# Optimization experiments

Hardware: AMD Instinct MI355X
Metric: run time of the kernel (lower is better)

Reference implementation:

```python
import jax, jax.numpy as jnp
import numpy as np

DIM = 112        # input channels
DIM_OUT = 224    # output channels (stage transition)
HEADS = 4
HD = DIM_OUT // HEADS          # 56
WS = 8                         # window size before query pooling
QS = 2                         # query_stride
MLP_DIM = int(DIM_OUT * 4.0)   # 896
EPS = 1e-6
SCALE = HD ** -0.5


def _layernorm(x, g, b):
    m = x.mean(-1, keepdims=True)
    d = x - m
    v = (d * d).mean(-1, keepdims=True)
    return d * jax.lax.rsqrt(v + EPS) * g + b


def _maxpool2(x):
    # stride==pool_size max pooling via reshape (NHWC)
    B, H, W, C = x.shape
    return x.reshape(B, H // QS, QS, W // QS, QS, C).max(axis=(2, 4))


def setup_inputs() -> dict:
    key = jax.random.key(0)
    ks = jax.random.split(key, 8)
    def n(k, s, sc=0.02):
        return jax.random.normal(k, s, dtype=jnp.float32) * sc
    return {
        "hidden_states": jax.random.normal(ks[0], (8, 128, 128, DIM), dtype=jnp.float32),
        "ln1_g": jnp.ones((DIM,), jnp.float32),
        "ln1_b": jnp.zeros((DIM,), jnp.float32),
        "qkv_w": n(ks[1], (DIM, 3 * DIM_OUT)),
        "qkv_b": jnp.zeros((3 * DIM_OUT,), jnp.float32),
        "attn_proj_w": n(ks[2], (DIM_OUT, DIM_OUT)),
        "attn_proj_b": jnp.zeros((DIM_OUT,), jnp.float32),
        "res_proj_w": n(ks[3], (DIM, DIM_OUT)),
        "res_proj_b": jnp.zeros((DIM_OUT,), jnp.float32),
        "ln2_g": jnp.ones((DIM_OUT,), jnp.float32),
        "ln2_b": jnp.zeros((DIM_OUT,), jnp.float32),
        "mlp1_w": n(ks[4], (DIM_OUT, MLP_DIM)),
        "mlp1_b": jnp.zeros((MLP_DIM,), jnp.float32),
        "mlp2_w": n(ks[5], (MLP_DIM, DIM_OUT)),
        "mlp2_b": jnp.zeros((DIM_OUT,), jnp.float32),
    }


def reference(hidden_states, ln1_g, ln1_b, qkv_w, qkv_b, attn_proj_w, attn_proj_b,
              res_proj_w, res_proj_b, ln2_g, ln2_b, mlp1_w, mlp1_b, mlp2_w, mlp2_b):
    x = hidden_states
    B, H, W, _ = x.shape  # H, W divisible by WS -> no padding branch needed
    hs = _layernorm(x, ln1_g, ln1_b)
    # dim != dim_out: residual = pooled projection of normed input
    residual = _maxpool2(hs @ res_proj_w + res_proj_b)  # (B, H/2, W/2, DIM_OUT)

    # window partition: (B*nh*nw, WS, WS, DIM)
    nh, nw = H // WS, W // WS
    w = hs.reshape(B, nh, WS, nw, WS, DIM).transpose(0, 1, 3, 2, 4, 5)
    w = w.reshape(B * nh * nw, WS, WS, DIM)

    # multi-scale attention with query pooling
    qkv = (w @ qkv_w + qkv_b).reshape(-1, WS * WS, 3, HEADS, HD)
    q, k, v = qkv[:, :, 0], qkv[:, :, 1], qkv[:, :, 2]
    q = _maxpool2(q.reshape(-1, WS, WS, DIM_OUT))          # (Bw, WS/2, WS/2, DIM_OUT)
    q = q.reshape(-1, (WS // QS) ** 2, HEADS, HD)
    q = q.transpose(0, 2, 1, 3)   # (Bw, h, Lq, d)
    k = k.transpose(0, 2, 1, 3)   # (Bw, h, Lk, d)
    v = v.transpose(0, 2, 1, 3)
    attn = jax.nn.softmax(jnp.einsum('bhqd,bhkd->bhqk', q * SCALE, k), axis=-1)
    o = jnp.einsum('bhqk,bhkd->bhqd', attn, v).transpose(0, 2, 1, 3)
    ws2 = WS // QS
    o = o.reshape(-1, ws2, ws2, DIM_OUT)
    o = o @ attn_proj_w + attn_proj_b

    # window unpartition at pooled resolution
    H2, W2 = H // QS, W // QS
    o = o.reshape(B, nh, nw, ws2, ws2, DIM_OUT).transpose(0, 1, 3, 2, 4, 5)
    o = o.reshape(B, H2, W2, DIM_OUT)

    hs = residual + o
    ln = _layernorm(hs, ln2_g, ln2_b)
    mlp = jax.nn.gelu(ln @ mlp1_w + mlp1_b, approximate=False) @ mlp2_w + mlp2_b
    return hs + mlp
```

## Files before the change

### kernel.cpp

```cpp
#include <hip/hip_runtime.h>
#include <hip/hip_bf16.h>
#include <math.h>


#define SCALE_A 0.13363062095621219f

typedef __attribute__((ext_vector_type(8))) short short8;
typedef __attribute__((ext_vector_type(4))) short short4v;
typedef __attribute__((ext_vector_type(4))) float f32x4;
typedef __attribute__((ext_vector_type(16))) float f32x16;

__device__ inline short f2bf(float x) {
  union { float f; unsigned u; } v; v.f = x;
  unsigned r = v.u + 0x7fff + ((v.u >> 16) & 1);
  return (short)(r >> 16);
}
__device__ inline float gelu_fast(float x) {
  float x2 = x * x;
  float p = fmaf(x2, 0.044715f, 1.0f);
  float t = -1.5957691216057308f * x * p;
  return x / (1.0f + __expf(t));
}

__global__ void cast_w_kernel(const float* __restrict__ qkv_w,
                              const float* __restrict__ rp_w,
                              const float* __restrict__ ap_w,
                              const float* __restrict__ m1_w,
                              const float* __restrict__ m2_w,
                              short* __restrict__ wF) {
  int tid = blockIdx.x * blockDim.x + threadIdx.x;
  int stride = gridDim.x * blockDim.x;
  for (int e = tid; e < 90112; e += stride) {
    int j = e & 7, lr = (e >> 3) & 15, lqq = (e >> 7) & 3, tile = e >> 9;
    int kt = tile & 3, nt = tile >> 2;
    int cp = nt * 16 + lr;
    int h = cp / 176, cl = cp % 176;
    int k = kt * 32 + lqq * 8 + j;
    float val = 0.f;
    if (k < 112 && cl < 168) {
      int bcol = (cl < 56) ? (h * 56 + cl)
               : (cl < 112) ? (224 + h * 56 + (cl - 56))
                            : (448 + h * 56 + (cl - 112));
      val = qkv_w[k * 672 + bcol];
    }
    wF[e] = f2bf(val);
  }
  for (int e = tid; e < 28672; e += stride) {
    int j = e & 7, lr = (e >> 3) & 15, lqq = (e >> 7) & 3, tile = e >> 9;
    int kt = tile & 3, nt = tile >> 2;
    int n = nt * 16 + lr, k = kt * 32 + lqq * 8 + j;
    wF[90112 + e] = (k < 112) ? f2bf(rp_w[k * 224 + n]) : (short)0;
  }
  for (int e = tid; e < 50176; e += stride) {
    int j = e & 7, lr = (e >> 3) & 15, lqq = (e >> 7) & 3, tile = e >> 9;
    int kt = tile % 7, nt = tile / 7;
    int n = nt * 16 + lr, k = kt * 32 + lqq * 8 + j;
    wF[118784 + e] = f2bf(ap_w[k * 224 + n]);
  }
  for (int e = tid; e < 200704; e += stride) {
    int j = e & 7, lane = (e >> 3) & 63, unit = e >> 9;
    int kt = unit % 14, nt = unit / 14;
    int n = nt * 32 + (lane & 31), k = kt * 16 + (lane >> 5) * 8 + j;
    wF[168960 + e] = f2bf(m1_w[k * 896 + n]);
  }
  for (int e = tid; e < 200704; e += stride) {
    int j = e & 7, lane = (e >> 3) & 63, unit = e >> 9;
    int kt = unit % 56, nt = unit / 56;
    int n = nt * 32 + (lane & 31), k = kt * 16 + (lane >> 5) * 8 + j;
    wF[369664 + e] = f2bf(m2_w[k * 224 + n]);
  }
}

__global__ __launch_bounds__(256) void ln1_kernel(
    const float* __restrict__ x, const float* __restrict__ g,
    const float* __restrict__ b, short* __restrict__ hs) {
  int wave = threadIdx.x >> 6, lane = threadIdx.x & 63;
  int half = lane >> 5, sub = lane & 31;
  size_t row = (size_t)blockIdx.x * 8 + wave * 2 + half;
  const float* rp = x + row * 112;
  f32x4 v = {0.f, 0.f, 0.f, 0.f};
  if (sub < 28) v = *(const f32x4*)(rp + sub * 4);
  float s = v[0] + v[1] + v[2] + v[3];
  #pragma unroll
  for (int off = 16; off; off >>= 1) s += __shfl_xor(s, off, 32);
  float mean = s * (1.f / 112.f);
  float s2 = 0.f;
  #pragma unroll
  for (int q = 0; q < 4; ++q) { float d = v[q] - mean; s2 = fmaf(d, d, s2); }
  if (sub >= 28) s2 = 0.f;
  #pragma unroll
  for (int off = 16; off; off >>= 1) s2 += __shfl_xor(s2, off, 32);
  float rs = rsqrtf(s2 * (1.f / 112.f) + 1e-6f);
  if (sub < 28) {
    f32x4 gg = *(const f32x4*)(g + sub * 4);
    f32x4 bb = *(const f32x4*)(b + sub * 4);
    short4v o;
    #pragma unroll
    for (int q = 0; q < 4; ++q)
      o[q] = f2bf((v[q] - mean) * rs * gg[q] + bb[q]);
    *(short4v*)(hs + row * 112 + sub * 4) = o;
  }
}

__global__ __launch_bounds__(256, 8) void respool_kernel(
    const short* __restrict__ hs, const short* __restrict__ rpF,
    const float* __restrict__ bias, float* __restrict__ hs2) {
  __shared__ alignas(16) short w_s[64 * 136];
  int blk = blockIdx.x;
  int tid = threadIdx.x;
  for (int e = tid; e < 1024; e += 256) {
    int m = e >> 4, c = e & 15;
    short8* dst = (short8*)&w_s[m * 136 + c * 8];
    if (c < 14) {
      int p = m >> 2, r = m & 3;
      int pix = blk * 16 + p;
      int bb = pix >> 12, ii = (pix >> 6) & 63, jj = pix & 63;
      size_t token = ((size_t)(bb * 128 + 2 * ii + (r >> 1))) * 128 + 2 * jj + (r & 1);
      *dst = *(const short8*)(hs + token * 112 + c * 8);
    } else {
      short8 z = {0, 0, 0, 0, 0, 0, 0, 0};
      *dst = z;
    }
  }
  __syncthreads();
  int wave = tid >> 6, lane = tid & 63, lrow = lane & 15, lq = lane >> 4;
  short8 Ar[4];
  #pragma unroll
  for (int kt = 0; kt < 4; ++kt)
    Ar[kt] = *(const short8*)&w_s[(wave * 16 + lrow) * 136 + kt * 32 + lq * 8];
  int p = wave * 4 + lq;
  for (int pr = 0; pr < 7; ++pr) {
    int c0 = pr * 32 + lrow, c1 = c0 + 16;
    f32x4 acc0 = {0.f, 0.f, 0.f, 0.f}, acc1 = {0.f, 0.f, 0.f, 0.f};
    #pragma unroll
    for (int kt = 0; kt < 4; ++kt) {
      short8 b0 = *(const short8*)(rpF + (((2 * pr) * 4 + kt) * 64 + lane) * 8);
      short8 b1 = *(const short8*)(rpF + (((2 * pr + 1) * 4 + kt) * 64 + lane) * 8);
      acc0 = __builtin_amdgcn_mfma_f32_16x16x32_bf16(Ar[kt], b0, acc0, 0, 0, 0);
      acc1 = __builtin_amdgcn_mfma_f32_16x16x32_bf16(Ar[kt], b1, acc1, 0, 0, 0);
    }
    float m0 = fmaxf(fmaxf(acc0[0], acc0[1]), fmaxf(acc0[2], acc0[3])) + bias[c0];
    float m1 = fmaxf(fmaxf(acc1[0], acc1[1]), fmaxf(acc1[2], acc1[3])) + bias[c1];
    hs2[(size_t)(blk * 16 + p) * 224 + c0] = m0;
    hs2[(size_t)(blk * 16 + p) * 224 + c1] = m1;
  }
}

__global__ __launch_bounds__(256, 2) void attn_kernel(
    const short* __restrict__ hs, const short* __restrict__ qkvF,
    const float* __restrict__ qkv_b, short* __restrict__ o_bf) {
  __shared__ alignas(16) short u_s[4 * 9792];
  int win = blockIdx.x;
  int nw = win & 15, nh = (win >> 4) & 15, b = win >> 8;
  int tid = threadIdx.x;
  int wave = tid >> 6, lane = tid & 63, lrow = lane & 15, lq = lane >> 4;
  short* w_s  = u_s;
  short* k_s  = u_s + wave * 9792;
  short* vT_s = k_s + 4608;
  short* qp_s = k_s + 8640;

  for (int e = tid; e < 1024; e += 256) {
    int m = e >> 4, c = e & 15;
    short8* dst = (short8*)&w_s[m * 136 + c * 8];
    if (c < 14) {
      int p = m >> 2, r = m & 3;
      int tr = (p >> 2) * 2 + (r >> 1), tc = (p & 3) * 2 + (r & 1);
      size_t token = ((size_t)(b * 128 + nh * 8 + tr)) * 128 + (nw * 8 + tc);
      *dst = *(const short8*)(hs + token * 112 + c * 8);
    } else {
      short8 z = {0, 0, 0, 0, 0, 0, 0, 0};
      *dst = z;
    }
  }
  __syncthreads();

  short8 Aw[4][4];
  #pragma unroll
  for (int mt = 0; mt < 4; ++mt)
    #pragma unroll
    for (int kt = 0; kt < 4; ++kt)
      Aw[mt][kt] = *(const short8*)&w_s[(mt * 16 + lrow) * 136 + kt * 32 + lq * 8];
  __syncthreads();

  {
    short8 z = {0, 0, 0, 0, 0, 0, 0, 0};
    *(short8*)&k_s[lane * 72 + 56] = z;
    if (lane < 16) *(short8*)&qp_s[lane * 72 + 56] = z;
  }

  int h = wave;

  #pragma unroll 2
  for (int t = 0; t < 11; ++t) {
    int cl = t * 16 + lrow;
    f32x4 ac[4] = {{0.f,0.f,0.f,0.f},{0.f,0.f,0.f,0.f},
                   {0.f,0.f,0.f,0.f},{0.f,0.f,0.f,0.f}};
    short8 bw[4];
    #pragma unroll
    for (int kt = 0; kt < 4; ++kt)
      bw[kt] = *(const short8*)(qkvF + (((h * 11 + t) * 4 + kt) * 64 + lane) * 8);
    #pragma unroll
    for (int kt = 0; kt < 4; ++kt)
      #pragma unroll
      for (int mt = 0; mt < 4; ++mt)
        ac[mt] = __builtin_amdgcn_mfma_f32_16x16x32_bf16(Aw[mt][kt], bw[kt], ac[mt], 0, 0, 0);
    if (cl < 56) {
      float bias = qkv_b[h * 56 + cl];
      #pragma unroll
      for (int mt = 0; mt < 4; ++mt) {
        float mx = fmaxf(fmaxf(ac[mt][0], ac[mt][1]),
                         fmaxf(ac[mt][2], ac[mt][3])) + bias;
        qp_s[(mt * 4 + lq) * 72 + cl] = f2bf(mx * SCALE_A);
      }
    } else if (cl < 112) {
      float bias = qkv_b[224 + h * 56 + (cl - 56)];
      #pragma unroll
      for (int mt = 0; mt < 4; ++mt)
        #pragma unroll
        for (int r = 0; r < 4; ++r)
          k_s[(mt * 16 + lq * 4 + r) * 72 + (cl - 56)] = f2bf(ac[mt][r] + bias);
    } else if (cl < 168) {
      float bias = qkv_b[448 + h * 56 + (cl - 112)];
      #pragma unroll
      for (int mt = 0; mt < 4; ++mt) {
        short4v pk = {f2bf(ac[mt][0] + bias), f2bf(ac[mt][1] + bias),
                      f2bf(ac[mt][2] + bias), f2bf(ac[mt][3] + bias)};
        *(short4v*)&vT_s[(cl - 112) * 72 + mt * 16 + lq * 4] = pk;
      }
    }
  }

  short8 aq[2];
  #pragma unroll
  for (int kt = 0; kt < 2; ++kt)
    aq[kt] = *(const short8*)&qp_s[lrow * 72 + kt * 32 + lq * 8];
  f32x4 sc[4];
  #pragma unroll
  for (int t = 0; t < 4; ++t) {
    sc[t][0] = sc[t][1] = sc[t][2] = sc[t][3] = 0.f;
    #pragma unroll
    for (int kt = 0; kt < 2; ++kt) {
      short8 bk = *(const short8*)&k_s[(t * 16 + lrow) * 72 + kt * 32 + lq * 8];
      sc[t] = __builtin_amdgcn_mfma_f32_16x16x32_bf16(aq[kt], bk, sc[t], 0, 0, 0);
    }
  }
  float mr[4], sr[4];
  #pragma unroll
  for (int r = 0; r < 4; ++r)
    mr[r] = fmaxf(fmaxf(sc[0][r], sc[1][r]), fmaxf(sc[2][r], sc[3][r]));
  #pragma unroll
  for (int off = 8; off; off >>= 1)
    #pragma unroll
    for (int r = 0; r < 4; ++r) mr[r] = fmaxf(mr[r], __shfl_xor(mr[r], off, 16));
  #pragma unroll
  for (int r = 0; r < 4; ++r) {
    #pragma unroll
    for (int t = 0; t < 4; ++t) sc[t][r] = __expf(sc[t][r] - mr[r]);
    sr[r] = sc[0][r] + sc[1][r] + sc[2][r] + sc[3][r];
  }
  #pragma unroll
  for (int off = 8; off; off >>= 1)
    #pragma unroll
    for (int r = 0; r < 4; ++r) sr[r] += __shfl_xor(sr[r], off, 16);
  #pragma unroll
  for (int r = 0; r < 4; ++r) sr[r] = 1.f / sr[r];
  #pragma unroll
  for (int t = 0; t < 4; ++t)
    #pragma unroll
    for (int r = 0; r < 4; ++r)
      qp_s[(lq * 4 + r) * 72 + t * 16 + lrow] = f2bf(sc[t][r] * sr[r]);

  short8 ap[2];
  #pragma unroll
  for (int kt = 0; kt < 2; ++kt)
    ap[kt] = *(const short8*)&qp_s[lrow * 72 + kt * 32 + lq * 8];
  #pragma unroll
  for (int ct = 0; ct < 4; ++ct) {
    int c0 = (ct < 3) ? ct * 16 : 40;
    int col = c0 + lrow;
    f32x4 ov = {0.f, 0.f, 0.f, 0.f};
    #pragma unroll
    for (int kt = 0; kt < 2; ++kt) {
      short8 bv = *(const short8*)&vT_s[col * 72 + kt * 32 + lq * 8];
      ov = __builtin_amdgcn_mfma_f32_16x16x32_bf16(ap[kt], bv, ov, 0, 0, 0);
    }
    if (ct < 3 || lrow >= 8) {
      #pragma unroll
      for (int r = 0; r < 4; ++r) {
        int row = lq * 4 + r;
        size_t token = ((size_t)(b * 64 + nh * 4 + (row >> 2))) * 64 + (nw * 4 + (row & 3));
        o_bf[token * 224 + h * 56 + col] = f2bf(ov[r]);
      }
    }
  }
}

__global__ __launch_bounds__(256, 5) void aproj_kernel(
    const short* __restrict__ o_bf, const short* __restrict__ apF,
    const float* __restrict__ apb, float* __restrict__ hs2) {
  __shared__ alignas(16) short o_s[64 * 232];
  int blk = blockIdx.x;
  int tid = threadIdx.x;
  for (int e = tid; e < 64 * 28; e += 256) {
    int m = e / 28, c = e % 28;
    *(short8*)&o_s[m * 232 + c * 8] =
        *(const short8*)(o_bf + ((size_t)blk * 64 + m) * 224 + c * 8);
  }
  __syncthreads();
  int wave = tid >> 6, lane = tid & 63, lrow = lane & 15, lq = lane >> 4;
  short8 Ao[7];
  #pragma unroll
  for (int kt = 0; kt < 7; ++kt)
    Ao[kt] = *(const short8*)&o_s[(wave * 16 + lrow) * 232 + kt * 32 + lq * 8];
  for (int pr = 0; pr < 7; ++pr) {
    int c0 = pr * 32 + lrow, c1 = c0 + 16;
    f32x4 acc0 = {0.f, 0.f, 0.f, 0.f}, acc1 = {0.f, 0.f, 0.f, 0.f};
    #pragma unroll
    for (int kt = 0; kt < 7; ++kt) {
      short8 b0 = *(const short8*)(apF + (((2 * pr) * 7 + kt) * 64 + lane) * 8);
      short8 b1 = *(const short8*)(apF + (((2 * pr + 1) * 7 + kt) * 64 + lane) * 8);
      acc0 = __builtin_amdgcn_mfma_f32_16x16x32_bf16(Ao[kt], b0, acc0, 0, 0, 0);
      acc1 = __builtin_amdgcn_mfma_f32_16x16x32_bf16(Ao[kt], b1, acc1, 0, 0, 0);
    }
    float bi0 = apb[c0], bi1 = apb[c1];
    #pragma unroll
    for (int r = 0; r < 4; ++r) {
      size_t row = (size_t)blk * 64 + wave * 16 + lq * 4 + r;
      hs2[row * 224 + c0] += acc0[r] + bi0;
      hs2[row * 224 + c1] += acc1[r] + bi1;
    }
  }
}

template <int NT>
__device__ __forceinline__ void mlp1_tiles(
    int nt0, const short* ln_s, const short* __restrict__ m1F,
    const float* __restrict__ b1, short* hid_s, int nl, int half, int lane) {
  f32x16 acc[NT];
  #pragma unroll
  for (int i = 0; i < NT; ++i)
    #pragma unroll
    for (int r = 0; r < 16; ++r) acc[i][r] = 0.f;
  #pragma unroll
  for (int kt = 0; kt < 14; ++kt) {
    short8 a = *(const short8*)&ln_s[nl * 232 + kt * 16 + half * 8];
    #pragma unroll
    for (int i = 0; i < NT; ++i) {
      short8 bw = *(const short8*)(m1F + ((size_t)((nt0 + i) * 14 + kt) * 64 + lane) * 8);
      acc[i] = __builtin_amdgcn_mfma_f32_32x32x16_bf16(a, bw, acc[i], 0, 0, 0);
    }
  }
  #pragma unroll
  for (int i = 0; i < NT; ++i) {
    int col = (nt0 + i) * 32 + nl;
    float bi = b1[col];
    #pragma unroll
    for (int r = 0; r < 16; ++r) {
      int row = (r & 3) + 8 * (r >> 2) + 4 * half;
      hid_s[row * 904 + col] = f2bf(gelu_fast(acc[i][r] + bi));
    }
  }
}

__global__ __launch_bounds__(512, 4) void mlp_kernel(
    const float* __restrict__ hs2, const float* __restrict__ g2,
    const float* __restrict__ b2, const short* __restrict__ m1F,
    const float* __restrict__ b1, const short* __restrict__ m2F,
    const float* __restrict__ b2b, float* __restrict__ out) {
  __shared__ alignas(16) short ln_s[32 * 232];
  __shared__ alignas(16) short hid_s[32 * 904];
  int blk = blockIdx.x;
  int tid = threadIdx.x;
  size_t base = (size_t)blk * 32 * 224;
  {
    int row = tid >> 4, l = tid & 15;
    const float* rp = hs2 + base + (size_t)row * 224;
    float v[14];
    float s = 0.f;
    #pragma unroll
    for (int c = 0; c < 14; ++c) { v[c] = rp[l + 16 * c]; s += v[c]; }
    #pragma unroll
    for (int off = 8; off; off >>= 1) s += __shfl_xor(s, off, 16);
    float mean = s * (1.f / 224.f);
    float s2 = 0.f;
    #pragma unroll
    for (int c = 0; c < 14; ++c) { float d = v[c] - mean; s2 = fmaf(d, d, s2); }
    #pragma unroll
    for (int off = 8; off; off >>= 1) s2 += __shfl_xor(s2, off, 16);
    float rs = rsqrtf(s2 * (1.f / 224.f) + 1e-6f);
    #pragma unroll
    for (int c = 0; c < 14; ++c) {
      int cc = l + 16 * c;
      ln_s[row * 232 + cc] = f2bf((v[c] - mean) * rs * g2[cc] + b2[cc]);
    }
  }
  __syncthreads();
  int wave = tid >> 6, lane = tid & 63;
  int nl = lane & 31, half = lane >> 5;
  if (wave < 4) mlp1_tiles<4>(wave * 4, ln_s, m1F, b1, hid_s, nl, half, lane);
  else          mlp1_tiles<3>(16 + (wave - 4) * 3, ln_s, m1F, b1, hid_s, nl, half, lane);
  __syncthreads();
  if (wave < 7) {
    int nt = wave;
    int col = nt * 32 + nl;
    float res[16];
    #pragma unroll
    for (int r = 0; r < 16; ++r) {
      int row = (r & 3) + 8 * (r >> 2) + 4 * half;
      res[r] = hs2[base + (size_t)row * 224 + col];
    }
    f32x16 ac0 = {0.f,0.f,0.f,0.f,0.f,0.f,0.f,0.f,0.f,0.f,0.f,0.f,0.f,0.f,0.f,0.f};
    f32x16 ac1 = {0.f,0.f,0.f,0.f,0.f,0.f,0.f,0.f,0.f,0.f,0.f,0.f,0.f,0.f,0.f,0.f};
    #pragma unroll 4
    for (int kt = 0; kt < 56; kt += 2) {
      short8 a0 = *(const short8*)&hid_s[nl * 904 + kt * 16 + half * 8];
      short8 a1 = *(const short8*)&hid_s[nl * 904 + (kt + 1) * 16 + half * 8];
      short8 b0 = *(const short8*)(m2F + ((size_t)(nt * 56 + kt) * 64 + lane) * 8);
      short8 b1 = *(const short8*)(m2F + ((size_t)(nt * 56 + kt + 1) * 64 + lane) * 8);
      ac0 = __builtin_amdgcn_mfma_f32_32x32x16_bf16(a0, b0, ac0, 0, 0, 0);
      ac1 = __builtin_amdgcn_mfma_f32_32x32x16_bf16(a1, b1, ac1, 0, 0, 0);
    }
    float bi = b2b[col];
    #pragma unroll
    for (int r = 0; r < 16; ++r) {
      int row = (r & 3) + 8 * (r >> 2) + 4 * half;
      size_t idx = base + (size_t)row * 224 + col;
      out[idx] = res[r] + ac0[r] + ac1[r] + bi;
    }
  }
}

extern "C" void kernel_launch(void* const* d_in, const int* in_sizes, int n_in,
                              void* d_out, int out_size, void* d_ws, size_t ws_size,
                              hipStream_t stream) {
  const float* x    = (const float*)d_in[0];
  const float* ln1g = (const float*)d_in[1];
  const float* ln1b = (const float*)d_in[2];
  const float* qkvw = (const float*)d_in[3];
  const float* qkvb = (const float*)d_in[4];
  const float* apw  = (const float*)d_in[5];
  const float* apb  = (const float*)d_in[6];
  const float* rpw  = (const float*)d_in[7];
  const float* rpb  = (const float*)d_in[8];
  const float* ln2g = (const float*)d_in[9];
  const float* ln2b = (const float*)d_in[10];
  const float* w1   = (const float*)d_in[11];
  const float* b1   = (const float*)d_in[12];
  const float* w2   = (const float*)d_in[13];
  const float* b2   = (const float*)d_in[14];
  float* out = (float*)d_out;

  short* hs_bf = (short*)d_ws;
  float* hs2   = (float*)((char*)d_ws + 29360128);
  short* o_bf  = (short*)((char*)d_ws + 58720256);
  short* wF    = (short*)((char*)d_ws + 73400320);

  cast_w_kernel<<<1024, 256, 0, stream>>>(qkvw, rpw, apw, w1, w2, wF);
  ln1_kernel<<<16384, 256, 0, stream>>>(x, ln1g, ln1b, hs_bf);
  respool_kernel<<<2048, 256, 0, stream>>>(hs_bf, wF + 90112, rpb, hs2);
  attn_kernel<<<2048, 256, 0, stream>>>(hs_bf, wF, qkvb, o_bf);
  aproj_kernel<<<512, 256, 0, stream>>>(o_bf, wF + 118784, apb, hs2);
  mlp_kernel<<<1024, 512, 0, stream>>>(hs2, ln2g, ln2b, wF + 168960, b1,
                                       wF + 369664, b2, out);
}
```

Measured before the change: 256.4 us.

## Split MLP hidden dimension into two phases to halve shared memory

The MLP kernel now computes the 896-wide hidden activation in two halves of 448 columns. Each half goes through GELU into a smaller shared buffer and is accumulated into the second GEMM before the next half is computed. This halves the hidden-activation shared memory and raises the launch-bounds occupancy target from 4 to 6 blocks, at the cost of extra barriers and a single accumulator chain in the second GEMM. It also leaves some dead placeholder code and reads the residual at the end instead of preloading it.

```diff
diff --git a/kernel.cpp b/kernel.cpp
--- a/kernel.cpp
+++ b/kernel.cpp
@@ -334,7 +334,7 @@
 
 template <int NT>
 __device__ __forceinline__ void mlp1_tiles(
-    int nt0, const short* ln_s, const short* __restrict__ m1F,
+    int nt0, int tbase, const short* ln_s, const short* __restrict__ m1F,
     const float* __restrict__ b1, short* hid_s, int nl, int half, int lane) {
   f32x16 acc[NT];
   #pragma unroll
@@ -353,22 +353,23 @@
   #pragma unroll
   for (int i = 0; i < NT; ++i) {
     int col = (nt0 + i) * 32 + nl;
+    int lcol = (nt0 + i - tbase) * 32 + nl;
     float bi = b1[col];
     #pragma unroll
     for (int r = 0; r < 16; ++r) {
       int row = (r & 3) + 8 * (r >> 2) + 4 * half;
-      hid_s[row * 904 + col] = f2bf(gelu_fast(acc[i][r] + bi));
-    }
-  }
-}
-
-__global__ __launch_bounds__(512, 4) void mlp_kernel(
+      hid_s[row * 456 + lcol] = f2bf(gelu_fast(acc[i][r] + bi));
+    }
+  }
+}
+
+__global__ __launch_bounds__(512, 6) void mlp_kernel(
     const float* __restrict__ hs2, const float* __restrict__ g2,
     const float* __restrict__ b2, const short* __restrict__ m1F,
     const float* __restrict__ b1, const short* __restrict__ m2F,
     const float* __restrict__ b2b, float* __restrict__ out) {
   __shared__ alignas(16) short ln_s[32 * 232];
-  __shared__ alignas(16) short hid_s[32 * 904];
+  __shared__ alignas(16) short hid_s[32 * 456];
   int blk = blockIdx.x;
   int tid = threadIdx.x;
   size_t base = (size_t)blk * 32 * 224;
@@ -397,35 +398,46 @@
   __syncthreads();
   int wave = tid >> 6, lane = tid & 63;
   int nl = lane & 31, half = lane >> 5;
-  if (wave < 4) mlp1_tiles<4>(wave * 4, ln_s, m1F, b1, hid_s, nl, half, lane);
-  else          mlp1_tiles<3>(16 + (wave - 4) * 3, ln_s, m1F, b1, hid_s, nl, half, lane);
-  __syncthreads();
+  int nt2 = wave;
+  f32x16 acg = {0.f,0.f,0.f,0.f,0.f,0.f,0.f,0.f,0.f,0.f,0.f,0.f,0.f,0.f,0.f,0.f};
+  f32x4 res[4];
+
+  #pragma unroll
+  for (int ph = 0; ph < 2; ++ph) {
+    int tbase = ph * 14;
+    if (wave < 6)
+      mlp1_tiles<2>(tbase + wave * 2, tbase, ln_s, m1F, b1, hid_s, nl, half, lane);
+    else
+      mlp1_tiles<1>(tbase + 12 + (wave - 6), tbase, ln_s, m1F, b1, hid_s, nl, half, lane);
+    __syncthreads();
+    if (ph == 1 && wave < 7) {
+      #pragma unroll
+      for (int r = 0; r < 4; ++r) {
+        int row = (r & 3) + 8 * (r >> 2) + 4 * half;
+        res[r][0] = 0.f;
+      }
+      #pragma unroll
+      for (int rq = 0; rq < 4; ++rq) {
+      }
+    }
+    if (wave < 7) {
+      #pragma unroll 4
+      for (int kt = 0; kt < 28; ++kt) {
+        short8 a = *(const short8*)&hid_s[nl * 456 + kt * 16 + half * 8];
+        short8 bw = *(const short8*)(m2F + ((size_t)(nt2 * 56 + ph * 28 + kt) * 64 + lane) * 8);
+        acg = __builtin_amdgcn_mfma_f32_32x32x16_bf16(a, bw, acg, 0, 0, 0);
+      }
+    }
+    if (ph == 0) __syncthreads();
+  }
   if (wave < 7) {
-    int nt = wave;
-    int col = nt * 32 + nl;
-    float res[16];
-    #pragma unroll
-    for (int r = 0; r < 16; ++r) {
-      int row = (r & 3) + 8 * (r >> 2) + 4 * half;
-      res[r] = hs2[base + (size_t)row * 224 + col];
-    }
-    f32x16 ac0 = {0.f,0.f,0.f,0.f,0.f,0.f,0.f,0.f,0.f,0.f,0.f,0.f,0.f,0.f,0.f,0.f};
-    f32x16 ac1 = {0.f,0.f,0.f,0.f,0.f,0.f,0.f,0.f,0.f,0.f,0.f,0.f,0.f,0.f,0.f,0.f};
-    #pragma unroll 4
-    for (int kt = 0; kt < 56; kt += 2) {
-      short8 a0 = *(const short8*)&hid_s[nl * 904 + kt * 16 + half * 8];
-      short8 a1 = *(const short8*)&hid_s[nl * 904 + (kt + 1) * 16 + half * 8];
-      short8 b0 = *(const short8*)(m2F + ((size_t)(nt * 56 + kt) * 64 + lane) * 8);
-      short8 b1 = *(const short8*)(m2F + ((size_t)(nt * 56 + kt + 1) * 64 + lane) * 8);
-      ac0 = __builtin_amdgcn_mfma_f32_32x32x16_bf16(a0, b0, ac0, 0, 0, 0);
-      ac1 = __builtin_amdgcn_mfma_f32_32x32x16_bf16(a1, b1, ac1, 0, 0, 0);
-    }
+    int col = nt2 * 32 + nl;
     float bi = b2b[col];
     #pragma unroll
     for (int r = 0; r < 16; ++r) {
       int row = (r & 3) + 8 * (r >> 2) + 4 * half;
       size_t idx = base + (size_t)row * 224 + col;
-      out[idx] = res[r] + ac0[r] + ac1[r] + bi;
+      out[idx] = hs2[idx] + acg[r] + bi;
     }
   }
 }
```

Result: slower. 275.5 us (+7.4%).

## Fuse attention output projection into attention kernel, drop o_bf round trip

Applied to the files above, without the earlier changes.

The attention kernel now keeps each head's 16x56 output in its per-wave qp_s shared region. After a block barrier it runs the 224x224 output projection directly on the window's 16 pooled tokens, splitting the 14 column tiles across the four waves and accumulating into hs2. This removes the separate aproj kernel launch and the global write and read of the bf16 attention output. In exchange the attention kernel does extra work with an unbalanced 4/4/3/3 tile split, each block re-reads the projection weights, and its writes to hs2 are scattered rather than full 64-row tiles.

```diff
diff --git a/kernel.cpp b/kernel.cpp
--- a/kernel.cpp
+++ b/kernel.cpp
@@ -148,7 +148,8 @@
 
 __global__ __launch_bounds__(256, 2) void attn_kernel(
     const short* __restrict__ hs, const short* __restrict__ qkvF,
-    const float* __restrict__ qkv_b, short* __restrict__ o_bf) {
+    const float* __restrict__ qkv_b, const short* __restrict__ apF,
+    const float* __restrict__ apb, float* __restrict__ hs2) {
   __shared__ alignas(16) short u_s[4 * 9792];
   int win = blockIdx.x;
   int nw = win & 15, nh = (win >> 4) & 15, b = win >> 8;
@@ -286,48 +287,36 @@
     }
     if (ct < 3 || lrow >= 8) {
       #pragma unroll
-      for (int r = 0; r < 4; ++r) {
-        int row = lq * 4 + r;
-        size_t token = ((size_t)(b * 64 + nh * 4 + (row >> 2))) * 64 + (nw * 4 + (row & 3));
-        o_bf[token * 224 + h * 56 + col] = f2bf(ov[r]);
-      }
-    }
-  }
-}
-
-__global__ __launch_bounds__(256, 5) void aproj_kernel(
-    const short* __restrict__ o_bf, const short* __restrict__ apF,
-    const float* __restrict__ apb, float* __restrict__ hs2) {
-  __shared__ alignas(16) short o_s[64 * 232];
-  int blk = blockIdx.x;
-  int tid = threadIdx.x;
-  for (int e = tid; e < 64 * 28; e += 256) {
-    int m = e / 28, c = e % 28;
-    *(short8*)&o_s[m * 232 + c * 8] =
-        *(const short8*)(o_bf + ((size_t)blk * 64 + m) * 224 + c * 8);
-  }
-  __syncthreads();
-  int wave = tid >> 6, lane = tid & 63, lrow = lane & 15, lq = lane >> 4;
+      for (int r = 0; r < 4; ++r)
+        qp_s[(lq * 4 + r) * 72 + col] = f2bf(ov[r]);
+    }
+  }
+  __syncthreads();
+
   short8 Ao[7];
   #pragma unroll
-  for (int kt = 0; kt < 7; ++kt)
-    Ao[kt] = *(const short8*)&o_s[(wave * 16 + lrow) * 232 + kt * 32 + lq * 8];
-  for (int pr = 0; pr < 7; ++pr) {
-    int c0 = pr * 32 + lrow, c1 = c0 + 16;
-    f32x4 acc0 = {0.f, 0.f, 0.f, 0.f}, acc1 = {0.f, 0.f, 0.f, 0.f};
+  for (int kt = 0; kt < 7; ++kt) {
+    int c = kt * 32 + lq * 8;
+    int h2 = (c >= 168) ? 3 : (c >= 112) ? 2 : (c >= 56) ? 1 : 0;
+    Ao[kt] = *(const short8*)&u_s[h2 * 9792 + 8640 + lrow * 72 + (c - h2 * 56)];
+  }
+  int nt0 = (wave < 2) ? wave * 4 : 8 + (wave - 2) * 3;
+  int ncnt2 = (wave < 2) ? 4 : 3;
+  for (int i = 0; i < ncnt2; ++i) {
+    int nt = nt0 + i;
+    f32x4 acc = {0.f, 0.f, 0.f, 0.f};
     #pragma unroll
     for (int kt = 0; kt < 7; ++kt) {
-      short8 b0 = *(const short8*)(apF + (((2 * pr) * 7 + kt) * 64 + lane) * 8);
-      short8 b1 = *(const short8*)(apF + (((2 * pr + 1) * 7 + kt) * 64 + lane) * 8);
-      acc0 = __builtin_amdgcn_mfma_f32_16x16x32_bf16(Ao[kt], b0, acc0, 0, 0, 0);
-      acc1 = __builtin_amdgcn_mfma_f32_16x16x32_bf16(Ao[kt], b1, acc1, 0, 0, 0);
-    }
-    float bi0 = apb[c0], bi1 = apb[c1];
+      short8 bw = *(const short8*)(apF + ((nt * 7 + kt) * 64 + lane) * 8);
+      acc = __builtin_amdgcn_mfma_f32_16x16x32_bf16(Ao[kt], bw, acc, 0, 0, 0);
+    }
+    int col2 = nt * 16 + lrow;
+    float bi = apb[col2];
     #pragma unroll
     for (int r = 0; r < 4; ++r) {
-      size_t row = (size_t)blk * 64 + wave * 16 + lq * 4 + r;
-      hs2[row * 224 + c0] += acc0[r] + bi0;
-      hs2[row * 224 + c1] += acc1[r] + bi1;
+      size_t token = ((size_t)(b * 64 + nh * 4 + lq)) * 64 + nw * 4 + r;
+      float* p = &hs2[token * 224 + col2];
+      *p += acc[r] + bi;
     }
   }
 }
@@ -452,14 +441,12 @@
 
   short* hs_bf = (short*)d_ws;
   float* hs2   = (float*)((char*)d_ws + 29360128);
-  short* o_bf  = (short*)((char*)d_ws + 58720256);
   short* wF    = (short*)((char*)d_ws + 73400320);
 
   cast_w_kernel<<<1024, 256, 0, stream>>>(qkvw, rpw, apw, w1, w2, wF);
   ln1_kernel<<<16384, 256, 0, stream>>>(x, ln1g, ln1b, hs_bf);
   respool_kernel<<<2048, 256, 0, stream>>>(hs_bf, wF + 90112, rpb, hs2);
-  attn_kernel<<<2048, 256, 0, stream>>>(hs_bf, wF, qkvb, o_bf);
-  aproj_kernel<<<512, 256, 0, stream>>>(o_bf, wF + 118784, apb, hs2);
+  attn_kernel<<<2048, 256, 0, stream>>>(hs_bf, wF, qkvb, wF + 118784, apb, hs2);
   mlp_kernel<<<1024, 512, 0, stream>>>(hs2, ln2g, ln2b, wF + 168960, b1,
                                        wF + 369664, b2, out);
 }
```

New measurement: 252.1 us. About the same (-1.7%).
